# Kernel tuning notes

Measured on AMD Instinct MI355X. Metric: run time of the kernel, lower is better.

Reference implementation:

```python
import jax, jax.numpy as jnp
import numpy as np

N_, E_, A_, B_, H_, DH_ = 8000, 12000, 48000, 64, 64, 4096
STEPS, POOL_ITERS = 4, 3

def rbf(x, K, cutoff):
    mu = jnp.linspace(0.0, cutoff, K).astype(x.dtype)
    gamma = 1.0 / (cutoff / (K - 1)) ** 2
    return jnp.exp(-gamma * (x[..., None] - mu) ** 2)

def gru_step(x, h, Wih, Whh, bih, bhh):
    gi = x @ Wih.T + bih
    gh = h @ Whh.T + bhh
    ir, iz, inew = jnp.split(gi, 3, axis=-1)
    hr, hz, hnew = jnp.split(gh, 3, axis=-1)
    r = jax.nn.sigmoid(ir + hr)
    z = jax.nn.sigmoid(iz + hz)
    n = jnp.tanh(inew + r * hnew)
    return (1.0 - z) * n + z * h

def lstm_step(x, h, c, Wih, Whh, bih, bhh):
    g = x @ Wih.T + bih + h @ Whh.T + bhh
    i, f, gg, o = jnp.split(g, 4, axis=-1)
    c2 = jax.nn.sigmoid(f) * c + jax.nn.sigmoid(i) * jnp.tanh(gg)
    h2 = jax.nn.sigmoid(o) * jnp.tanh(c2)
    return h2, c2

def seg_softmax(e, seg, num_seg):
    m = jax.ops.segment_max(e, seg, num_segments=num_seg)
    ex = jnp.exp(e - m[seg])
    s = jax.ops.segment_sum(ex, seg, num_segments=num_seg)
    return ex / s[seg]

def _forward(node_attribute, edge_attribute, edge_length, angle, edge_src, edge_dst, angle_src, angle_dst, graph_ids, projW, projb, bondW, bondb, efW, efb, gnn_b, buW, bub, auW, aub, gWih, gWhh, gbih, gbhh, sWih0, sWhh0, sbih0, sbhh0, sWih1, sWhh1, sbih1, sbhh1, spW, spb, prelu_a):
    N, E = node_attribute.shape[0], edge_src.shape[0]
    x0 = jax.nn.relu(node_attribute @ projW + projb)  # [N, H]
    len_rbf = rbf(edge_length, 8, 4.0)                # [E, 8]
    edge_feat = jnp.concatenate([edge_attribute, len_rbf], axis=-1)  # [E, 16]
    ee_feat = jnp.concatenate([rbf(angle, 8, float(np.pi)), len_rbf[angle_src]], axis=-1)  # [A, 16]
    Wb = (edge_feat @ bondW + bondb).reshape(E, H_, H_)  # per-bond weight matrices (constant over steps)
    Wa = (ee_feat @ efW + efb).reshape(-1, H_, H_)       # per-angle weight matrices
    nf, hid = x0, x0
    for _ in range(STEPS):
        bm = nf[edge_src]                                # gather src node feats per bond [E, H]
        ha = jax.nn.relu(bm @ auW + aub)                 # angle_update
        m_ang = jnp.einsum('ai,aio->ao', ha[angle_src], Wa)  # [A, H]
        amsg = jax.ops.segment_sum(m_ang, angle_dst, num_segments=E)  # scatter-sum to bonds
        hb = jax.nn.relu(bm @ buW + bub) + amsg          # bond_update + angle message
        m = jnp.einsum('ei,eio->eo', hb, Wb)             # [E, H]
        nf = jax.nn.relu(jax.ops.segment_sum(m, edge_dst, num_segments=N) + gnn_b)
        nf = gru_step(nf, hid, gWih, gWhh, gbih, gbhh)   # 1-step, 1-layer GRU: output == new hidden
        hid = nf
    agg = jnp.concatenate([nf, x0], axis=-1)             # [N, 2H]
    D = agg.shape[-1]
    q_star = jnp.zeros((B_, 2 * D), agg.dtype)
    h0 = jnp.zeros((B_, D), agg.dtype); c0 = h0
    h1 = h0; c1 = h0
    for _ in range(POOL_ITERS):                          # Set2Set
        h0, c0 = lstm_step(q_star, h0, c0, sWih0, sWhh0, sbih0, sbhh0)
        h1, c1 = lstm_step(h0, h1, c1, sWih1, sWhh1, sbih1, sbhh1)
        q = h1                                           # [B, D]
        e = jnp.sum(agg * q[graph_ids], axis=-1)         # [N]
        alpha = seg_softmax(e, graph_ids, B_)
        readout = jax.ops.segment_sum(alpha[:, None] * agg, graph_ids, num_segments=B_)
        q_star = jnp.concatenate([q, readout], axis=-1)  # [B, 2D]
    out = q_star @ spW + spb                             # [B, DH]
    return jnp.where(out >= 0, out, prelu_a * out)       # PReLU

def setup_inputs():
    key = jax.random.key(0)
    ks = jax.random.split(key, 40)
    r = lambda i, shape, s=1.0: s * jax.random.normal(ks[i], shape, jnp.float32)
    inp = {}
    inp['node_attribute'] = r(0, (N_, 110))
    inp['edge_attribute'] = r(1, (E_, 8))
    inp['edge_length'] = jax.random.uniform(ks[2], (E_,), jnp.float32, 0.5, 4.0)
    inp['angle'] = jax.random.uniform(ks[3], (A_,), jnp.float32, 0.0, float(np.pi))
    inp['edge_src'] = jax.random.randint(ks[4], (E_,), 0, N_)
    inp['edge_dst'] = jax.random.randint(ks[5], (E_,), 0, N_)
    inp['angle_src'] = jax.random.randint(ks[6], (A_,), 0, E_)
    inp['angle_dst'] = jax.random.randint(ks[7], (A_,), 0, E_)
    inp['graph_ids'] = jnp.sort(jax.random.randint(ks[8], (N_,), 0, B_))
    w = 0.05
    inp['projW'] = r(9, (110, H_), w); inp['projb'] = jnp.zeros((H_,), jnp.float32)
    inp['bondW'] = r(10, (16, H_ * H_), w); inp['bondb'] = jnp.zeros((H_ * H_,), jnp.float32)
    inp['efW'] = r(11, (16, H_ * H_), w); inp['efb'] = jnp.zeros((H_ * H_,), jnp.float32)
    inp['gnn_b'] = jnp.zeros((H_,), jnp.float32)
    inp['buW'] = r(12, (H_, H_), w); inp['bub'] = jnp.zeros((H_,), jnp.float32)
    inp['auW'] = r(13, (H_, H_), w); inp['aub'] = jnp.zeros((H_,), jnp.float32)
    inp['gWih'] = r(14, (3 * H_, H_), w); inp['gWhh'] = r(15, (3 * H_, H_), w)
    inp['gbih'] = jnp.zeros((3 * H_,), jnp.float32); inp['gbhh'] = jnp.zeros((3 * H_,), jnp.float32)
    D = 2 * H_  # Set2Set feature dim = 128
    inp['sWih0'] = r(16, (4 * D, 2 * D), w); inp['sWhh0'] = r(17, (4 * D, D), w)
    inp['sbih0'] = jnp.zeros((4 * D,), jnp.float32); inp['sbhh0'] = jnp.zeros((4 * D,), jnp.float32)
    inp['sWih1'] = r(18, (4 * D, D), w); inp['sWhh1'] = r(19, (4 * D, D), w)
    inp['sbih1'] = jnp.zeros((4 * D,), jnp.float32); inp['sbhh1'] = jnp.zeros((4 * D,), jnp.float32)
    inp['spW'] = r(20, (4 * H_, DH_), w); inp['spb'] = jnp.zeros((DH_,), jnp.float32)
    inp['prelu_a'] = jnp.full((1,), 0.25, jnp.float32)
    return inp

def reference(node_attribute, edge_attribute, edge_length, angle, edge_src, edge_dst, angle_src, angle_dst, graph_ids, projW, projb, bondW, bondb, efW, efb, gnn_b, buW, bub, auW, aub, gWih, gWhh, gbih, gbhh, sWih0, sWhh0, sbih0, sbhh0, sWih1, sWhh1, sbih1, sbhh1, spW, spb, prelu_a):
    return _forward(node_attribute, edge_attribute, edge_length, angle, edge_src, edge_dst, angle_src, angle_dst, graph_ids, projW, projb, bondW, bondb, efW, efb, gnn_b, buW, bub, auW, aub, gWih, gWhh, gbih, gbhh, sWih0, sWhh0, sbih0, sbhh0, sWih1, sWhh1, sbih1, sbhh1, spW, spb, prelu_a)
```

## Files before the change

kernel.cpp:

```cpp
#include <hip/hip_runtime.h>
#include <math.h>

#define N_N 8000
#define N_E 12000
#define N_A 48000
#define N_B 64
#define N_H 64
#define N_DH 4096

typedef _Float16 h16;
typedef __attribute__((ext_vector_type(8))) _Float16 h16x8;
typedef __attribute__((ext_vector_type(4))) float f32x4;

__device__ __forceinline__ float atomAddF(float* p, float v) {
  return __hip_atomic_fetch_add(p, v, __ATOMIC_RELAXED, __HIP_MEMORY_SCOPE_AGENT);
}
__device__ __forceinline__ float sigm(float x) { return 1.f / (1.f + expf(-x)); }

#define SB_PROJ 2000
#define SB_FEAT (SB_PROJ + 235)
#define SB_PREP (SB_FEAT + 704)
#define SB_BND  (SB_PREP + 32)
#define SB_ZERO (SB_BND + 1330)
#define PREP_B0 32768
#define PREP_B1 (PREP_B0 + 69632)
#define PREP_B2 (PREP_B1 + 69632)
#define PREP_B3 (PREP_B2 + 4096)
#define PREP_B4 (PREP_B3 + 4096)

__global__ __launch_bounds__(256) void k_setup(
    const float* __restrict__ na, const float* __restrict__ projW,
    const float* __restrict__ projb, const float* __restrict__ ea,
    const float* __restrict__ el, const float* __restrict__ ang,
    const int* __restrict__ asrc, const int* __restrict__ gid,
    const float* __restrict__ gWih, const float* __restrict__ gWhh,
    const float* __restrict__ efW, const float* __restrict__ efb,
    const float* __restrict__ bondW, const float* __restrict__ bondb,
    const float* __restrict__ auW, const float* __restrict__ buW,
    float* __restrict__ x0, float* __restrict__ ef, float* __restrict__ ee,
    int* __restrict__ gstart, int* __restrict__ gend,
    h16* __restrict__ W3t, h16* __restrict__ ttA, h16* __restrict__ ttB,
    h16* __restrict__ wtAU, h16* __restrict__ wtBU,
    float4* __restrict__ amsg0_4, float4* __restrict__ nacc0_4,
    float4* __restrict__ qz_4) {
  int bx = blockIdx.x, tid = threadIdx.x;
  if (bx < SB_PROJ) {
    int wid = bx * 4 + (tid >> 6);
    int lane = tid & 63;
    if (wid < N_N) {
      const float* row = na + (size_t)wid * 110;
      float acc = projb[lane];
      for (int k = 0; k < 110; ++k) acc = fmaf(row[k], projW[k * 64 + lane], acc);
      x0[(size_t)wid * 64 + lane] = fmaxf(acc, 0.f);
    }
  } else if (bx < SB_FEAT) {
    int i = (bx - SB_PROJ) * 256 + tid;
    const float g2 = (7.f / 4.f) * (7.f / 4.f);
    if (i < N_E) {
      int e = i;
      float x = el[e];
#pragma unroll
      for (int j = 0; j < 8; ++j) ef[e * 16 + j] = ea[e * 8 + j];
#pragma unroll
      for (int j = 0; j < 8; ++j) {
        float d = x - j * (4.f / 7.f);
        ef[e * 16 + 8 + j] = expf(-g2 * d * d);
      }
    } else if (i < N_E + N_A) {
      int a = i - N_E;
      const float PIf = 3.14159265358979323846f;
      float x = ang[a];
      float g1 = (7.f / PIf) * (7.f / PIf);
#pragma unroll
      for (int j = 0; j < 8; ++j) {
        float d = x - j * (PIf / 7.f);
        ee[a * 16 + j] = expf(-g1 * d * d);
      }
      float y = el[asrc[a]];
#pragma unroll
      for (int j = 0; j < 8; ++j) {
        float d = y - j * (4.f / 7.f);
        ee[a * 16 + 8 + j] = expf(-g2 * d * d);
      }
    }
  } else if (bx < SB_PREP) {
    int i = (bx - SB_FEAT) * 256 + tid;
    if (i < PREP_B0) {
      int col = i >> 7, k = i & 127;
      int grp = col >> 6, u = col & 63;
      float v;
      if (grp == 0) v = (k < 64) ? gWih[u * 64 + k] : gWhh[u * 64 + k - 64];
      else if (grp == 1) v = (k < 64) ? gWih[(64 + u) * 64 + k] : gWhh[(64 + u) * 64 + k - 64];
      else if (grp == 2) v = (k < 64) ? gWih[(128 + u) * 64 + k] : 0.f;
      else v = (k < 64) ? 0.f : gWhh[(128 + u) * 64 + k - 64];
      W3t[i] = (h16)v;
    } else if (i < PREP_B1) {
      int j = i - PREP_B0;
      int n = j >> 6, i2 = j & 63;
      int k = n >> 6, o = n & 63;
      float val = (k < 16) ? efW[(size_t)k * 4096 + i2 * 64 + o] : efb[i2 * 64 + o];
      ttA[j] = (h16)val;
    } else if (i < PREP_B2) {
      int j = i - PREP_B1;
      int n = j >> 6, i2 = j & 63;
      int k = n >> 6, o = n & 63;
      float val = (k < 16) ? bondW[(size_t)k * 4096 + i2 * 64 + o] : bondb[i2 * 64 + o];
      ttB[j] = (h16)val;
    } else if (i < PREP_B3) {
      int j = i - PREP_B2;
      int o = j >> 6, i2 = j & 63;
      wtAU[j] = (h16)auW[i2 * 64 + o];
    } else if (i < PREP_B4) {
      int j = i - PREP_B3;
      int o = j >> 6, i2 = j & 63;
      wtBU[j] = (h16)buW[i2 * 64 + o];
    }
  } else if (bx < SB_BND) {
    int n = (bx - SB_PREP) * 256 + tid;
    if (n < N_N) {
      int g = gid[n];
      if (n == 0 || gid[n - 1] != g) gstart[g] = n;
      if (n == N_N - 1 || gid[n + 1] != g) gend[g] = n + 1;
    }
  } else if (bx < SB_ZERO) {
    int i = (bx - SB_BND) * 256 + tid;
    float4 z = (float4){0.f, 0.f, 0.f, 0.f};
    if (i < 192000) amsg0_4[i] = z;
    else if (i < 320000) nacc0_4[i - 192000] = z;
    else if (i < 340480) qz_4[i - 320000] = z;
  }
}

template <bool ANGLE>
__global__ __launch_bounds__(256) void k_fused_mm(
    const float* __restrict__ xcur, const int* __restrict__ map,
    const int* __restrict__ esrc, const h16* __restrict__ WtU,
    const float* __restrict__ biasU, const float* __restrict__ amsg_in,
    const float* __restrict__ feat, const h16* __restrict__ Tt,
    const int* __restrict__ dst, float* __restrict__ outacc, int T,
    float4* __restrict__ zbuf, int zcount4) {
  if (zbuf && blockIdx.y == 0) {
    int stride = gridDim.x * 256;
    for (int i = blockIdx.x * 256 + threadIdx.x; i < zcount4; i += stride)
      zbuf[i] = (float4){0.f, 0.f, 0.f, 0.f};
  }
  __shared__ h16 haT[4][2048];
  __shared__ float f_lds[128 * 17];
  __shared__ int dst_lds[128];
  int tid = threadIdx.x;
  int base = blockIdx.x * 128;
  int oc = blockIdx.y;
  for (int e = tid; e < 128 * 16; e += 256) {
    int il = e >> 4, k = e & 15;
    int g = base + il;
    if (g >= T) g = T - 1;
    f_lds[il * 17 + k] = feat[(size_t)g * 16 + k];
  }
  if (tid < 128) {
    int g = base + tid;
    if (g >= T) g = T - 1;
    dst_lds[tid] = dst[g];
  }
  __syncthreads();

  int wave = tid >> 6, lane = tid & 63;
  int l15 = lane & 15, lq = lane >> 4;
  int ibl = wave * 32;
  int ib0 = base + ibl;
  h16* myT = haT[wave];

  {
    h16x8 xafr[2][2];
#pragma unroll
    for (int s = 0; s < 2; ++s) {
      int item = ib0 + s * 16 + l15;
      if (item >= T) item = T - 1;
      int e = ANGLE ? map[item] : item;
      const float* vp = xcur + (size_t)esrc[e] * 64;
#pragma unroll
      for (int ks = 0; ks < 2; ++ks) {
        const float4* p = (const float4*)(vp + ks * 32 + 8 * lq);
        float4 v0 = p[0], v1 = p[1];
        h16x8 a;
        a[0] = (h16)v0.x; a[1] = (h16)v0.y; a[2] = (h16)v0.z; a[3] = (h16)v0.w;
        a[4] = (h16)v1.x; a[5] = (h16)v1.y; a[6] = (h16)v1.z; a[7] = (h16)v1.w;
        xafr[s][ks] = a;
      }
    }
    f32x4 aU[2][4];
#pragma unroll
    for (int s = 0; s < 2; ++s)
#pragma unroll
      for (int nt = 0; nt < 4; ++nt) aU[s][nt] = (f32x4){0.f, 0.f, 0.f, 0.f};
#pragma unroll
    for (int nt = 0; nt < 4; ++nt) {
#pragma unroll
      for (int ks = 0; ks < 2; ++ks) {
        h16x8 b = *(const h16x8*)(WtU + (size_t)(nt * 16 + l15) * 64 + ks * 32 + 8 * lq);
#pragma unroll
        for (int s = 0; s < 2; ++s)
          aU[s][nt] = __builtin_amdgcn_mfma_f32_16x16x32_f16(xafr[s][ks], b, aU[s][nt], 0, 0, 0);
      }
    }
#pragma unroll
    for (int s = 0; s < 2; ++s) {
#pragma unroll
      for (int nt = 0; nt < 4; ++nt) {
        int o = nt * 16 + l15;
        float bo = biasU[o];
#pragma unroll
        for (int r = 0; r < 4; ++r) {
          int row = s * 16 + lq * 4 + r;
          float val = fmaxf(aU[s][nt][r] + bo, 0.f);
          if (!ANGLE) {
            int item = ib0 + row;
            if (item >= T) item = T - 1;
            val += amsg_in[(size_t)item * 64 + o];
          }
          int idx = (((row * 64 + o) << 1) ^ ((row & 7) << 4)) >> 1;
          myT[idx] = (h16)val;
        }
      }
    }
  }

  h16x8 afr[2][2];
#pragma unroll
  for (int s = 0; s < 2; ++s) {
#pragma unroll
    for (int ks = 0; ks < 2; ++ks) {
      int row = s * 16 + l15;
      int byte = ((row * 64 + ks * 32 + 8 * lq) << 1) ^ ((row & 7) << 4);
      afr[s][ks] = *(const h16x8*)((const char*)myT + byte);
    }
  }

  f32x4 acc[2][2];
#pragma unroll
  for (int s = 0; s < 2; ++s)
#pragma unroll
    for (int nt = 0; nt < 2; ++nt) acc[s][nt] = (f32x4){0.f, 0.f, 0.f, 0.f};

  for (int kk = 0; kk < 16; ++kk) {
    h16x8 bfr[2][2];
#pragma unroll
    for (int nt = 0; nt < 2; ++nt)
#pragma unroll
      for (int ks = 0; ks < 2; ++ks)
        bfr[nt][ks] = *(const h16x8*)(Tt + (size_t)(kk * 64 + (oc * 2 + nt) * 16 + l15) * 64 +
                                      ks * 32 + 8 * lq);
    h16x8 a2[2][2];
#pragma unroll
    for (int s = 0; s < 2; ++s) {
      h16 fs = (h16)f_lds[(ibl + s * 16 + l15) * 17 + kk];
      a2[s][0] = afr[s][0] * fs;
      a2[s][1] = afr[s][1] * fs;
    }
#pragma unroll
    for (int s = 0; s < 2; ++s)
#pragma unroll
      for (int nt = 0; nt < 2; ++nt)
#pragma unroll
        for (int ks = 0; ks < 2; ++ks)
          acc[s][nt] = __builtin_amdgcn_mfma_f32_16x16x32_f16(a2[s][ks], bfr[nt][ks],
                                                              acc[s][nt], 0, 0, 0);
  }
  {
    h16x8 bfr[2][2];
#pragma unroll
    for (int nt = 0; nt < 2; ++nt)
#pragma unroll
      for (int ks = 0; ks < 2; ++ks)
        bfr[nt][ks] = *(const h16x8*)(Tt + (size_t)(16 * 64 + (oc * 2 + nt) * 16 + l15) * 64 +
                                      ks * 32 + 8 * lq);
#pragma unroll
    for (int s = 0; s < 2; ++s)
#pragma unroll
      for (int nt = 0; nt < 2; ++nt)
#pragma unroll
        for (int ks = 0; ks < 2; ++ks)
          acc[s][nt] = __builtin_amdgcn_mfma_f32_16x16x32_f16(afr[s][ks], bfr[nt][ks],
                                                              acc[s][nt], 0, 0, 0);
  }

#pragma unroll
  for (int s = 0; s < 2; ++s) {
#pragma unroll
    for (int r = 0; r < 4; ++r) {
      int il = ibl + s * 16 + lq * 4 + r;
      int item = base + il;
      if (item < T) {
        float* op = outacc + (size_t)dst_lds[il] * 64;
#pragma unroll
        for (int nt = 0; nt < 2; ++nt)
          atomAddF(op + (oc * 2 + nt) * 16 + l15, acc[s][nt][r]);
      }
    }
  }
}

__global__ __launch_bounds__(256) void k_gru2(
    const float* __restrict__ nacc, const float* __restrict__ gnnb,
    const float* __restrict__ h, const h16* __restrict__ W3t,
    const float* __restrict__ gbih, const float* __restrict__ gbhh,
    float* __restrict__ hout, const float* __restrict__ x0,
    float* __restrict__ agg, int wagg, float4* __restrict__ zbuf, int zcount4) {
  if (zbuf) {
    int stride = gridDim.x * 256;
    for (int i = blockIdx.x * 256 + threadIdx.x; i < zcount4; i += stride)
      zbuf[i] = (float4){0.f, 0.f, 0.f, 0.f};
  }
  int tid = threadIdx.x, wave = tid >> 6, lane = tid & 63;
  int l15 = lane & 15, lq = lane >> 4;
  int ib0 = blockIdx.x * 64 + wave * 16;
  int nodeA = ib0 + l15;
  if (nodeA >= N_N) nodeA = N_N - 1;

  h16x8 afr[4];
#pragma unroll
  for (int ks = 0; ks < 2; ++ks) {
    const float4* p = (const float4*)(nacc + (size_t)nodeA * 64 + ks * 32 + 8 * lq);
    const float4* gp = (const float4*)(gnnb + ks * 32 + 8 * lq);
    float4 v0 = p[0], v1 = p[1], g0 = gp[0], g1 = gp[1];
    h16x8 a;
    a[0] = (h16)fmaxf(v0.x + g0.x, 0.f); a[1] = (h16)fmaxf(v0.y + g0.y, 0.f);
    a[2] = (h16)fmaxf(v0.z + g0.z, 0.f); a[3] = (h16)fmaxf(v0.w + g0.w, 0.f);
    a[4] = (h16)fmaxf(v1.x + g1.x, 0.f); a[5] = (h16)fmaxf(v1.y + g1.y, 0.f);
    a[6] = (h16)fmaxf(v1.z + g1.z, 0.f); a[7] = (h16)fmaxf(v1.w + g1.w, 0.f);
    afr[ks] = a;
  }
#pragma unroll
  for (int ks = 0; ks < 2; ++ks) {
    const float4* p = (const float4*)(h + (size_t)nodeA * 64 + ks * 32 + 8 * lq);
    float4 v0 = p[0], v1 = p[1];
    h16x8 a;
    a[0] = (h16)v0.x; a[1] = (h16)v0.y; a[2] = (h16)v0.z; a[3] = (h16)v0.w;
    a[4] = (h16)v1.x; a[5] = (h16)v1.y; a[6] = (h16)v1.z; a[7] = (h16)v1.w;
    afr[2 + ks] = a;
  }

  f32x4 acc[16];
#pragma unroll
  for (int nt = 0; nt < 16; ++nt) acc[nt] = (f32x4){0.f, 0.f, 0.f, 0.f};
#pragma unroll
  for (int nt = 0; nt < 16; ++nt) {
#pragma unroll
    for (int ks = 0; ks < 4; ++ks) {
      if (nt >= 8 && nt < 12 && ks >= 2) continue;
      if (nt >= 12 && ks < 2) continue;
      h16x8 b = *(const h16x8*)(W3t + (size_t)(nt * 16 + l15) * 128 + ks * 32 + 8 * lq);
      acc[nt] = __builtin_amdgcn_mfma_f32_16x16x32_f16(afr[ks], b, acc[nt], 0, 0, 0);
    }
  }

#pragma unroll
  for (int nt0 = 0; nt0 < 4; ++nt0) {
    int u = nt0 * 16 + l15;
    float br = gbih[u] + gbhh[u];
    float bz = gbih[64 + u] + gbhh[64 + u];
    float bin_ = gbih[128 + u];
    float bhn = gbhh[128 + u];
#pragma unroll
    for (int r = 0; r < 4; ++r) {
      int node = ib0 + lq * 4 + r;
      if (node < N_N) {
        float rr = sigm(acc[nt0][r] + br);
        float zz = sigm(acc[nt0 + 4][r] + bz);
        float nn = tanhf(acc[nt0 + 8][r] + bin_ + rr * (acc[nt0 + 12][r] + bhn));
        float hv = h[(size_t)node * 64 + u];
        float val = (1.f - zz) * nn + zz * hv;
        hout[(size_t)node * 64 + u] = val;
        if (wagg) {
          agg[(size_t)node * 128 + u] = val;
          agg[(size_t)node * 128 + 64 + u] = x0[(size_t)node * 64 + u];
        }
      }
    }
  }
}


__global__ __launch_bounds__(256) void k_lstm2(
    const float* __restrict__ x, int xdim,
    const float* __restrict__ hin, const float* __restrict__ cin,
    const float* __restrict__ Wih, const float* __restrict__ Whh,
    const float* __restrict__ bih, const float* __restrict__ bhh,
    float* __restrict__ hout, float* __restrict__ cout) {
  int w = (blockIdx.x * blockDim.x + threadIdx.x) >> 6;
  int lane = threadIdx.x & 63;
  if (w >= N_B * 128) return;
  int b = w >> 7, u = w & 127;
  float a0 = 0.f, a1 = 0.f, a2 = 0.f, a3 = 0.f;
  const float* xr = x + (size_t)b * xdim;
  for (int k = lane; k < xdim; k += 64) {
    float xv = xr[k];
    a0 = fmaf(xv, Wih[(size_t)u * xdim + k], a0);
    a1 = fmaf(xv, Wih[(size_t)(128 + u) * xdim + k], a1);
    a2 = fmaf(xv, Wih[(size_t)(256 + u) * xdim + k], a2);
    a3 = fmaf(xv, Wih[(size_t)(384 + u) * xdim + k], a3);
  }
  const float* hr = hin + (size_t)b * 128;
#pragma unroll
  for (int k0 = 0; k0 < 128; k0 += 64) {
    int k = k0 + lane;
    float hv = hr[k];
    a0 = fmaf(hv, Whh[(size_t)u * 128 + k], a0);
    a1 = fmaf(hv, Whh[(size_t)(128 + u) * 128 + k], a1);
    a2 = fmaf(hv, Whh[(size_t)(256 + u) * 128 + k], a2);
    a3 = fmaf(hv, Whh[(size_t)(384 + u) * 128 + k], a3);
  }
#pragma unroll
  for (int m = 1; m < 64; m <<= 1) {
    a0 += __shfl_xor(a0, m);
    a1 += __shfl_xor(a1, m);
    a2 += __shfl_xor(a2, m);
    a3 += __shfl_xor(a3, m);
  }
  if (lane == 0) {
    float gi = a0 + bih[u] + bhh[u];
    float gf = a1 + bih[128 + u] + bhh[128 + u];
    float gg = a2 + bih[256 + u] + bhh[256 + u];
    float go = a3 + bih[384 + u] + bhh[384 + u];
    float c2 = sigm(gf) * cin[(size_t)b * 128 + u] + sigm(gi) * tanhf(gg);
    hout[(size_t)b * 128 + u] = sigm(go) * tanhf(c2);
    cout[(size_t)b * 128 + u] = c2;
  }
}

__global__ __launch_bounds__(256) void k_pool2(
    const float* __restrict__ agg, const int* __restrict__ gstart,
    const int* __restrict__ gend, const float* __restrict__ q,
    float* __restrict__ q_star) {
  int g = blockIdx.x;
  int s = gstart[g], t = gend[g];
  int cnt = t - s;
  if (cnt < 0) cnt = 0;
  if (cnt > 1024) cnt = 1024;
  __shared__ float ew[1024];
  __shared__ float red[8];
  __shared__ float comb[256];
  int tid = threadIdx.x, wave = tid >> 6, lane = tid & 63;
  float qa = q[g * 128 + lane], qb = q[g * 128 + 64 + lane];
  for (int i = wave; i < cnt; i += 4) {
    int n = s + i;
    float a = agg[(size_t)n * 128 + lane] * qa + agg[(size_t)n * 128 + 64 + lane] * qb;
#pragma unroll
    for (int m = 1; m < 64; m <<= 1) a += __shfl_xor(a, m);
    if (lane == 0) ew[i] = a;
  }
  __syncthreads();
  float mx = -INFINITY;
  for (int i = tid; i < cnt; i += 256) mx = fmaxf(mx, ew[i]);
#pragma unroll
  for (int m = 1; m < 64; m <<= 1) mx = fmaxf(mx, __shfl_xor(mx, m));
  if (lane == 0) red[wave] = mx;
  __syncthreads();
  mx = fmaxf(fmaxf(red[0], red[1]), fmaxf(red[2], red[3]));
  float sm = 0.f;
  for (int i = tid; i < cnt; i += 256) sm += expf(ew[i] - mx);
#pragma unroll
  for (int m = 1; m < 64; m <<= 1) sm += __shfl_xor(sm, m);
  if (lane == 0) red[4 + wave] = sm;
  __syncthreads();
  sm = red[4] + red[5] + red[6] + red[7];
  float inv = (sm > 0.f) ? 1.f / sm : 0.f;
  __syncthreads();
  for (int i = tid; i < cnt; i += 256) ew[i] = expf(ew[i] - mx) * inv;
  __syncthreads();
  int d = tid & 127, half = tid >> 7;
  float acc = 0.f;
  for (int i = half; i < cnt; i += 2)
    acc = fmaf(ew[i], agg[(size_t)(s + i) * 128 + d], acc);
  comb[tid] = acc;
  __syncthreads();
  if (half == 0) {
    float r2 = acc + comb[128 + tid];
    q_star[(size_t)g * 256 + d] = q[(size_t)g * 128 + d];
    q_star[(size_t)g * 256 + 128 + d] = r2;
  }
}

__global__ void k_out(const float* __restrict__ qs, const float* __restrict__ W,
                      const float* __restrict__ bias, const float* __restrict__ pa,
                      float* __restrict__ out) {
  int idx = blockIdx.x * blockDim.x + threadIdx.x;
  if (idx >= N_B * N_DH) return;
  int b = idx >> 12, d = idx & 4095;
  float acc = bias[d];
  const float* q = qs + (size_t)b * 256;
  for (int k = 0; k < 256; ++k) acc = fmaf(q[k], W[(size_t)k * 4096 + d], acc);
  float a = pa[0];
  out[idx] = acc >= 0.f ? acc : a * acc;
}

enum : size_t {
  OFF_X0 = 0,
  OFF_HA = OFF_X0 + (size_t)N_N * 64,
  OFF_HB = OFF_HA + (size_t)N_N * 64,
  OFF_EF = OFF_HB + (size_t)N_N * 64,
  OFF_EE = OFF_EF + (size_t)N_E * 16,
  OFF_AMSG0 = OFF_EE + (size_t)N_A * 16,
  OFF_AMSG1 = OFF_AMSG0 + (size_t)N_E * 64,
  OFF_NACC0 = OFF_AMSG1 + (size_t)N_E * 64,
  OFF_NACC1 = OFF_NACC0 + (size_t)N_N * 64,
  OFF_AGG = OFF_NACC1 + (size_t)N_N * 64,
  OFF_QSTAR = OFF_AGG + (size_t)N_N * 128,
  OFF_H0A = OFF_QSTAR + N_B * 256,
  OFF_H0B = OFF_H0A + N_B * 128,
  OFF_C0A = OFF_H0B + N_B * 128,
  OFF_C0B = OFF_C0A + N_B * 128,
  OFF_H1A = OFF_C0B + N_B * 128,
  OFF_H1B = OFF_H1A + N_B * 128,
  OFF_C1A = OFF_H1B + N_B * 128,
  OFF_C1B = OFF_C1A + N_B * 128,
  OFF_GSTART = OFF_C1B + N_B * 128,
  OFF_GEND = OFF_GSTART + N_B,
  OFF_TT_ANG = (OFF_GEND + N_B + 63) & ~(size_t)63,
  OFF_TT_BOND = OFF_TT_ANG + 34816,
  OFF_WT_AU = OFF_TT_BOND + 34816,
  OFF_WT_BU = OFF_WT_AU + 2048,
  OFF_W3T = OFF_WT_BU + 2048,
  WS_FLOATS = OFF_W3T + 16384
};

extern "C" void kernel_launch(void* const* d_in, const int* in_sizes, int n_in,
                              void* d_out, int out_size, void* d_ws, size_t ws_size,
                              hipStream_t stream) {
  (void)in_sizes; (void)n_in; (void)out_size; (void)ws_size;
  const float* na    = (const float*)d_in[0];
  const float* ea    = (const float*)d_in[1];
  const float* el    = (const float*)d_in[2];
  const float* ang   = (const float*)d_in[3];
  const int*   esrc  = (const int*)d_in[4];
  const int*   edst  = (const int*)d_in[5];
  const int*   asrc  = (const int*)d_in[6];
  const int*   adst  = (const int*)d_in[7];
  const int*   gid   = (const int*)d_in[8];
  const float* projW = (const float*)d_in[9];
  const float* projb = (const float*)d_in[10];
  const float* bondW = (const float*)d_in[11];
  const float* bondb = (const float*)d_in[12];
  const float* efW   = (const float*)d_in[13];
  const float* efb   = (const float*)d_in[14];
  const float* gnnb  = (const float*)d_in[15];
  const float* buW   = (const float*)d_in[16];
  const float* bub   = (const float*)d_in[17];
  const float* auW   = (const float*)d_in[18];
  const float* aub   = (const float*)d_in[19];
  const float* gWih  = (const float*)d_in[20];
  const float* gWhh  = (const float*)d_in[21];
  const float* gbih  = (const float*)d_in[22];
  const float* gbhh  = (const float*)d_in[23];
  const float* sWih0 = (const float*)d_in[24];
  const float* sWhh0 = (const float*)d_in[25];
  const float* sbih0 = (const float*)d_in[26];
  const float* sbhh0 = (const float*)d_in[27];
  const float* sWih1 = (const float*)d_in[28];
  const float* sWhh1 = (const float*)d_in[29];
  const float* sbih1 = (const float*)d_in[30];
  const float* sbhh1 = (const float*)d_in[31];
  const float* spW   = (const float*)d_in[32];
  const float* spb   = (const float*)d_in[33];
  const float* pa    = (const float*)d_in[34];
  float* out = (float*)d_out;
  float* ws = (float*)d_ws;

  float* x0    = ws + OFF_X0;
  float* hA    = ws + OFF_HA;
  float* hB    = ws + OFF_HB;
  float* ef    = ws + OFF_EF;
  float* ee    = ws + OFF_EE;
  float* amsg0 = ws + OFF_AMSG0;
  float* amsg1 = ws + OFF_AMSG1;
  float* nacc0 = ws + OFF_NACC0;
  float* nacc1 = ws + OFF_NACC1;
  float* agg   = ws + OFF_AGG;
  float* qstar = ws + OFF_QSTAR;
  float* h0a = ws + OFF_H0A; float* h0b = ws + OFF_H0B;
  float* c0a = ws + OFF_C0A; float* c0b = ws + OFF_C0B;
  float* h1a = ws + OFF_H1A; float* h1b = ws + OFF_H1B;
  float* c1a = ws + OFF_C1A; float* c1b = ws + OFF_C1B;
  int* gstart = (int*)(ws + OFF_GSTART);
  h16* ttA = (h16*)(ws + OFF_TT_ANG);
  h16* ttB = (h16*)(ws + OFF_TT_BOND);
  h16* wtAU = (h16*)(ws + OFF_WT_AU);
  h16* wtBU = (h16*)(ws + OFF_WT_BU);
  h16* w3t  = (h16*)(ws + OFF_W3T);

  hipMemsetAsync(gstart, 0x7f, 2 * N_B * sizeof(int), stream);
  k_setup<<<SB_ZERO, 256, 0, stream>>>(
      na, projW, projb, ea, el, ang, asrc, gid, gWih, gWhh, efW, efb, bondW, bondb,
      auW, buW, x0, ef, ee, gstart, gstart + N_B, w3t, ttA, ttB, wtAU, wtBU,
      (float4*)amsg0, (float4*)nacc0, (float4*)qstar);

  const float* cur = x0;
  float* bufs[2] = {hA, hB};
  float* amsgs[2] = {amsg0, amsg1};
  float* naccs[2] = {nacc0, nacc1};
  for (int s = 0; s < 4; ++s) {
    float* amsg_c = amsgs[s & 1];
    float* amsg_o = amsgs[(s + 1) & 1];
    float* nacc_c = naccs[s & 1];
    float* nacc_o = naccs[(s + 1) & 1];
    k_fused_mm<true><<<dim3((N_A + 127) / 128, 2), 256, 0, stream>>>(
        cur, asrc, esrc, wtAU, aub, nullptr, ee, ttA, adst, amsg_c, N_A,
        nullptr, 0);
    k_fused_mm<false><<<dim3((N_E + 127) / 128, 2), 256, 0, stream>>>(
        cur, nullptr, esrc, wtBU, bub, amsg_c, ef, ttB, edst, nacc_c, N_E,
        (float4*)amsg_o, N_E * 64 / 4);
    float* nxt = bufs[s & 1];
    k_gru2<<<(N_N + 63) / 64, 256, 0, stream>>>(nacc_c, gnnb, cur, w3t, gbih, gbhh,
                                                nxt, x0, agg, (s == 3) ? 1 : 0,
                                                (float4*)nacc_o, N_N * 64 / 4);
    cur = nxt;
  }

  float *h0i = h0a, *h0o = h0b, *c0i = c0a, *c0o = c0b;
  float *h1i = h1a, *h1o = h1b, *c1i = c1a, *c1o = c1b;
  for (int it = 0; it < 3; ++it) {
    k_lstm2<<<(N_B * 128 * 64 + 255) / 256, 256, 0, stream>>>(
        qstar, 256, h0i, c0i, sWih0, sWhh0, sbih0, sbhh0, h0o, c0o);
    k_lstm2<<<(N_B * 128 * 64 + 255) / 256, 256, 0, stream>>>(
        h0o, 128, h1i, c1i, sWih1, sWhh1, sbih1, sbhh1, h1o, c1o);
    k_pool2<<<N_B, 256, 0, stream>>>(agg, gstart, gstart + N_B, h1o, qstar);
    float* tmp;
    tmp = h0i; h0i = h0o; h0o = tmp;
    tmp = c0i; c0i = c0o; c0o = tmp;
    tmp = h1i; h1i = h1o; h1o = tmp;
    tmp = c1i; c1i = c1o; c1o = tmp;
  }
  k_out<<<(N_B * N_DH + 255) / 256, 256, 0, stream>>>(qstar, spW, spb, pa, out);
}
```

Baseline: 414.4 us.

## Factor angle messages per-edge, split bond kernel, fuse Set2Set into one kernel

```diff
diff --git a/kernel.cpp b/kernel.cpp
--- a/kernel.cpp
+++ b/kernel.cpp
@@ -18,31 +18,37 @@
 __device__ __forceinline__ float sigm(float x) { return 1.f / (1.f + expf(-x)); }
 
 #define SB_PROJ 2000
-#define SB_FEAT (SB_PROJ + 235)
-#define SB_PREP (SB_FEAT + 704)
+#define SB_FEAT (SB_PROJ + 47)
+#define SB_PREP (SB_FEAT + 1984)
 #define SB_BND  (SB_PREP + 32)
-#define SB_ZERO (SB_BND + 1330)
+#define SB_END  (SB_BND + 1250)
 #define PREP_B0 32768
 #define PREP_B1 (PREP_B0 + 69632)
 #define PREP_B2 (PREP_B1 + 69632)
 #define PREP_B3 (PREP_B2 + 4096)
 #define PREP_B4 (PREP_B3 + 4096)
+#define PREP_B5 (PREP_B4 + 131072)
+#define PREP_B6 (PREP_B5 + 65536)
+#define PREP_B7 (PREP_B6 + 65536)
+#define PREP_B8 (PREP_B7 + 65536)
 
 __global__ __launch_bounds__(256) void k_setup(
     const float* __restrict__ na, const float* __restrict__ projW,
     const float* __restrict__ projb, const float* __restrict__ ea,
-    const float* __restrict__ el, const float* __restrict__ ang,
-    const int* __restrict__ asrc, const int* __restrict__ gid,
+    const float* __restrict__ el, const int* __restrict__ gid,
     const float* __restrict__ gWih, const float* __restrict__ gWhh,
     const float* __restrict__ efW, const float* __restrict__ efb,
     const float* __restrict__ bondW, const float* __restrict__ bondb,
     const float* __restrict__ auW, const float* __restrict__ buW,
-    float* __restrict__ x0, float* __restrict__ ef, float* __restrict__ ee,
+    const float* __restrict__ sWih0, const float* __restrict__ sWhh0,
+    const float* __restrict__ sWih1, const float* __restrict__ sWhh1,
+    float* __restrict__ x0, float* __restrict__ ef,
     int* __restrict__ gstart, int* __restrict__ gend,
     h16* __restrict__ W3t, h16* __restrict__ ttA, h16* __restrict__ ttB,
     h16* __restrict__ wtAU, h16* __restrict__ wtBU,
-    float4* __restrict__ amsg0_4, float4* __restrict__ nacc0_4,
-    float4* __restrict__ qz_4) {
+    float* __restrict__ w0xT, float* __restrict__ w0hT,
+    float* __restrict__ w1xT, float* __restrict__ w1hT,
+    float4* __restrict__ amsg0_4, float4* __restrict__ nacc0_4) {
   int bx = blockIdx.x, tid = threadIdx.x;
   if (bx < SB_PROJ) {
     int wid = bx * 4 + (tid >> 6);
@@ -54,10 +60,9 @@
       x0[(size_t)wid * 64 + lane] = fmaxf(acc, 0.f);
     }
   } else if (bx < SB_FEAT) {
-    int i = (bx - SB_PROJ) * 256 + tid;
-    const float g2 = (7.f / 4.f) * (7.f / 4.f);
-    if (i < N_E) {
-      int e = i;
+    int e = (bx - SB_PROJ) * 256 + tid;
+    if (e < N_E) {
+      const float g2 = (7.f / 4.f) * (7.f / 4.f);
       float x = el[e];
 #pragma unroll
       for (int j = 0; j < 8; ++j) ef[e * 16 + j] = ea[e * 8 + j];
@@ -65,22 +70,6 @@
       for (int j = 0; j < 8; ++j) {
         float d = x - j * (4.f / 7.f);
         ef[e * 16 + 8 + j] = expf(-g2 * d * d);
-      }
-    } else if (i < N_E + N_A) {
-      int a = i - N_E;
-      const float PIf = 3.14159265358979323846f;
-      float x = ang[a];
-      float g1 = (7.f / PIf) * (7.f / PIf);
-#pragma unroll
-      for (int j = 0; j < 8; ++j) {
-        float d = x - j * (PIf / 7.f);
-        ee[a * 16 + j] = expf(-g1 * d * d);
-      }
-      float y = el[asrc[a]];
-#pragma unroll
-      for (int j = 0; j < 8; ++j) {
-        float d = y - j * (4.f / 7.f);
-        ee[a * 16 + 8 + j] = expf(-g2 * d * d);
       }
     }
   } else if (bx < SB_PREP) {
@@ -114,6 +103,22 @@
       int j = i - PREP_B3;
       int o = j >> 6, i2 = j & 63;
       wtBU[j] = (h16)buW[i2 * 64 + o];
+    } else if (i < PREP_B5) {
+      int j = i - PREP_B4;
+      int k = j >> 9, r = j & 511;
+      w0xT[j] = sWih0[(size_t)r * 256 + k];
+    } else if (i < PREP_B6) {
+      int j = i - PREP_B5;
+      int k = j >> 9, r = j & 511;
+      w0hT[j] = sWhh0[(size_t)r * 128 + k];
+    } else if (i < PREP_B7) {
+      int j = i - PREP_B6;
+      int k = j >> 9, r = j & 511;
+      w1xT[j] = sWih1[(size_t)r * 128 + k];
+    } else if (i < PREP_B8) {
+      int j = i - PREP_B7;
+      int k = j >> 9, r = j & 511;
+      w1hT[j] = sWhh1[(size_t)r * 128 + k];
     }
   } else if (bx < SB_BND) {
     int n = (bx - SB_PREP) * 256 + tid;
@@ -122,51 +127,35 @@
       if (n == 0 || gid[n - 1] != g) gstart[g] = n;
       if (n == N_N - 1 || gid[n + 1] != g) gend[g] = n + 1;
     }
-  } else if (bx < SB_ZERO) {
+  } else if (bx < SB_END) {
     int i = (bx - SB_BND) * 256 + tid;
     float4 z = (float4){0.f, 0.f, 0.f, 0.f};
     if (i < 192000) amsg0_4[i] = z;
     else if (i < 320000) nacc0_4[i - 192000] = z;
-    else if (i < 340480) qz_4[i - 320000] = z;
   }
 }
 
-template <bool ANGLE>
-__global__ __launch_bounds__(256) void k_fused_mm(
-    const float* __restrict__ xcur, const int* __restrict__ map,
-    const int* __restrict__ esrc, const h16* __restrict__ WtU,
-    const float* __restrict__ biasU, const float* __restrict__ amsg_in,
-    const float* __restrict__ feat, const h16* __restrict__ Tt,
-    const int* __restrict__ dst, float* __restrict__ outacc, int T,
-    float4* __restrict__ zbuf, int zcount4) {
-  if (zbuf && blockIdx.y == 0) {
-    int stride = gridDim.x * 256;
-    for (int i = blockIdx.x * 256 + threadIdx.x; i < zcount4; i += stride)
-      zbuf[i] = (float4){0.f, 0.f, 0.f, 0.f};
-  }
+__global__ __launch_bounds__(256) void k_edgeP(
+    const float* __restrict__ xcur, const int* __restrict__ esrc,
+    const h16* __restrict__ wtAU, const float* __restrict__ aub,
+    const h16* __restrict__ ttA, const float* __restrict__ ef,
+    h16* __restrict__ P8, float* __restrict__ Q) {
   __shared__ h16 haT[4][2048];
-  __shared__ float f_lds[128 * 17];
-  __shared__ int dst_lds[128];
-  int tid = threadIdx.x;
+  __shared__ float f_lds[128 * 9];
+  int tid = threadIdx.x, wave = tid >> 6, lane = tid & 63;
+  int l15 = lane & 15, lq = lane >> 4;
+  int oc = blockIdx.y;
   int base = blockIdx.x * 128;
-  int oc = blockIdx.y;
-  for (int e = tid; e < 128 * 16; e += 256) {
-    int il = e >> 4, k = e & 15;
-    int g = base + il;
-    if (g >= T) g = T - 1;
-    f_lds[il * 17 + k] = feat[(size_t)g * 16 + k];
-  }
-  if (tid < 128) {
-    int g = base + tid;
-    if (g >= T) g = T - 1;
-    dst_lds[tid] = dst[g];
-  }
-  __syncthreads();
-
-  int wave = tid >> 6, lane = tid & 63;
-  int l15 = lane & 15, lq = lane >> 4;
-  int ibl = wave * 32;
-  int ib0 = base + ibl;
+  if (oc >= 2) {
+    for (int e2 = tid; e2 < 128 * 8; e2 += 256) {
+      int il = e2 >> 3, k = e2 & 7;
+      int g = base + il;
+      if (g >= N_E) g = N_E - 1;
+      f_lds[il * 9 + k] = ef[(size_t)g * 16 + 8 + k];
+    }
+    __syncthreads();
+  }
+  int ibl = wave * 32, ib0 = base + ibl;
   h16* myT = haT[wave];
 
   {
@@ -174,9 +163,8 @@
 #pragma unroll
     for (int s = 0; s < 2; ++s) {
       int item = ib0 + s * 16 + l15;
-      if (item >= T) item = T - 1;
-      int e = ANGLE ? map[item] : item;
-      const float* vp = xcur + (size_t)esrc[e] * 64;
+      if (item >= N_E) item = N_E - 1;
+      const float* vp = xcur + (size_t)esrc[item] * 64;
 #pragma unroll
       for (int ks = 0; ks < 2; ++ks) {
         const float4* p = (const float4*)(vp + ks * 32 + 8 * lq);
@@ -193,62 +181,241 @@
 #pragma unroll
       for (int nt = 0; nt < 4; ++nt) aU[s][nt] = (f32x4){0.f, 0.f, 0.f, 0.f};
 #pragma unroll
-    for (int nt = 0; nt < 4; ++nt) {
+    for (int nt = 0; nt < 4; ++nt)
 #pragma unroll
       for (int ks = 0; ks < 2; ++ks) {
-        h16x8 b = *(const h16x8*)(WtU + (size_t)(nt * 16 + l15) * 64 + ks * 32 + 8 * lq);
+        h16x8 b = *(const h16x8*)(wtAU + (size_t)(nt * 16 + l15) * 64 + ks * 32 + 8 * lq);
 #pragma unroll
         for (int s = 0; s < 2; ++s)
           aU[s][nt] = __builtin_amdgcn_mfma_f32_16x16x32_f16(xafr[s][ks], b, aU[s][nt], 0, 0, 0);
       }
-    }
-#pragma unroll
-    for (int s = 0; s < 2; ++s) {
+#pragma unroll
+    for (int s = 0; s < 2; ++s)
 #pragma unroll
       for (int nt = 0; nt < 4; ++nt) {
         int o = nt * 16 + l15;
-        float bo = biasU[o];
+        float bo = aub[o];
 #pragma unroll
         for (int r = 0; r < 4; ++r) {
           int row = s * 16 + lq * 4 + r;
           float val = fmaxf(aU[s][nt][r] + bo, 0.f);
-          if (!ANGLE) {
-            int item = ib0 + row;
-            if (item >= T) item = T - 1;
-            val += amsg_in[(size_t)item * 64 + o];
-          }
           int idx = (((row * 64 + o) << 1) ^ ((row & 7) << 4)) >> 1;
           myT[idx] = (h16)val;
         }
       }
-    }
-  }
-
+  }
   h16x8 afr[2][2];
 #pragma unroll
-  for (int s = 0; s < 2; ++s) {
+  for (int s = 0; s < 2; ++s)
 #pragma unroll
     for (int ks = 0; ks < 2; ++ks) {
       int row = s * 16 + l15;
       int byte = ((row * 64 + ks * 32 + 8 * lq) << 1) ^ ((row & 7) << 4);
       afr[s][ks] = *(const h16x8*)((const char*)myT + byte);
     }
-  }
-
-  f32x4 acc[2][2];
+
+  if (oc < 2) {
+#pragma unroll
+    for (int kk = oc * 4; kk < oc * 4 + 4; ++kk) {
+      f32x4 acc[2][4];
+#pragma unroll
+      for (int s = 0; s < 2; ++s)
+#pragma unroll
+        for (int nt = 0; nt < 4; ++nt) acc[s][nt] = (f32x4){0.f, 0.f, 0.f, 0.f};
+#pragma unroll
+      for (int nt = 0; nt < 4; ++nt)
+#pragma unroll
+        for (int ks = 0; ks < 2; ++ks) {
+          h16x8 b = *(const h16x8*)(ttA + (size_t)(kk * 64 + nt * 16 + l15) * 64 +
+                                    ks * 32 + 8 * lq);
+#pragma unroll
+          for (int s = 0; s < 2; ++s)
+            acc[s][nt] = __builtin_amdgcn_mfma_f32_16x16x32_f16(afr[s][ks], b, acc[s][nt], 0, 0, 0);
+        }
+#pragma unroll
+      for (int s = 0; s < 2; ++s)
+#pragma unroll
+        for (int r = 0; r < 4; ++r) {
+          int e = ib0 + s * 16 + lq * 4 + r;
+          if (e < N_E) {
+#pragma unroll
+            for (int nt = 0; nt < 4; ++nt)
+              P8[((size_t)e * 8 + kk) * 64 + nt * 16 + l15] = (h16)acc[s][nt][r];
+          }
+        }
+    }
+  } else {
+    int no = oc - 2;
+    f32x4 qacc[2][2];
+#pragma unroll
+    for (int s = 0; s < 2; ++s)
+#pragma unroll
+      for (int nt = 0; nt < 2; ++nt) qacc[s][nt] = (f32x4){0.f, 0.f, 0.f, 0.f};
+    for (int kk = 8; kk < 16; ++kk) {
+      h16x8 a2[2][2];
+#pragma unroll
+      for (int s = 0; s < 2; ++s) {
+        h16 fs = (h16)f_lds[(ibl + s * 16 + l15) * 9 + (kk - 8)];
+        a2[s][0] = afr[s][0] * fs;
+        a2[s][1] = afr[s][1] * fs;
+      }
+#pragma unroll
+      for (int nt = 0; nt < 2; ++nt)
+#pragma unroll
+        for (int ks = 0; ks < 2; ++ks) {
+          h16x8 b = *(const h16x8*)(ttA + (size_t)(kk * 64 + (no * 2 + nt) * 16 + l15) * 64 +
+                                    ks * 32 + 8 * lq);
+#pragma unroll
+          for (int s = 0; s < 2; ++s)
+            qacc[s][nt] = __builtin_amdgcn_mfma_f32_16x16x32_f16(a2[s][ks], b, qacc[s][nt], 0, 0, 0);
+        }
+    }
+#pragma unroll
+    for (int nt = 0; nt < 2; ++nt)
+#pragma unroll
+      for (int ks = 0; ks < 2; ++ks) {
+        h16x8 b = *(const h16x8*)(ttA + (size_t)(16 * 64 + (no * 2 + nt) * 16 + l15) * 64 +
+                                  ks * 32 + 8 * lq);
+#pragma unroll
+        for (int s = 0; s < 2; ++s)
+          qacc[s][nt] = __builtin_amdgcn_mfma_f32_16x16x32_f16(afr[s][ks], b, qacc[s][nt], 0, 0, 0);
+      }
+#pragma unroll
+    for (int s = 0; s < 2; ++s)
+#pragma unroll
+      for (int r = 0; r < 4; ++r) {
+        int e = ib0 + s * 16 + lq * 4 + r;
+        if (e < N_E) {
+#pragma unroll
+          for (int nt = 0; nt < 2; ++nt)
+            Q[(size_t)e * 64 + (no * 2 + nt) * 16 + l15] = qacc[s][nt][r];
+        }
+      }
+  }
+}
+
+__global__ __launch_bounds__(256) void k_angle(
+    const float* __restrict__ ang, const int* __restrict__ asrc,
+    const int* __restrict__ adst, const h16* __restrict__ P8,
+    const float* __restrict__ Q, float* __restrict__ amsg) {
+  int w = (blockIdx.x * blockDim.x + threadIdx.x) >> 6;
+  int lane = threadIdx.x & 63;
+  if (w >= N_A) return;
+  float x = ang[w];
+  int e = asrc[w], d = adst[w];
+  float acc = Q[(size_t)e * 64 + lane];
+  const h16* p = P8 + (size_t)e * 512;
+  const float PIf = 3.14159265358979323846f;
+  const float g1 = (7.f / PIf) * (7.f / PIf);
+#pragma unroll
+  for (int j = 0; j < 8; ++j) {
+    float dd = x - j * (PIf / 7.f);
+    acc = fmaf(expf(-g1 * dd * dd), (float)p[j * 64 + lane], acc);
+  }
+  atomAddF(amsg + (size_t)d * 64 + lane, acc);
+}
+
+__global__ __launch_bounds__(256) void k_bond(
+    const float* __restrict__ xcur, const int* __restrict__ esrc,
+    const h16* __restrict__ wtBU, const float* __restrict__ bub,
+    const float* __restrict__ amsg_in, const float* __restrict__ ef,
+    const h16* __restrict__ ttB, const int* __restrict__ edst,
+    float* __restrict__ nacc, float4* __restrict__ zbuf, int zcount4) {
+  if (blockIdx.y == 0) {
+    int stride = gridDim.x * 256;
+    for (int i = blockIdx.x * 256 + threadIdx.x; i < zcount4; i += stride)
+      zbuf[i] = (float4){0.f, 0.f, 0.f, 0.f};
+  }
+  __shared__ h16 haT[4][2048];
+  __shared__ float f_lds[128 * 17];
+  __shared__ int dst_lds[128];
+  int tid = threadIdx.x;
+  int base = blockIdx.x * 128;
+  int oc = blockIdx.y;
+  for (int e2 = tid; e2 < 128 * 16; e2 += 256) {
+    int il = e2 >> 4, k = e2 & 15;
+    int g = base + il;
+    if (g >= N_E) g = N_E - 1;
+    f_lds[il * 17 + k] = ef[(size_t)g * 16 + k];
+  }
+  if (tid < 128) {
+    int g = base + tid;
+    if (g >= N_E) g = N_E - 1;
+    dst_lds[tid] = edst[g];
+  }
+  __syncthreads();
+
+  int wave = tid >> 6, lane = tid & 63;
+  int l15 = lane & 15, lq = lane >> 4;
+  int ibl = wave * 32, ib0 = base + ibl;
+  h16* myT = haT[wave];
+
+  {
+    h16x8 xafr[2][2];
+#pragma unroll
+    for (int s = 0; s < 2; ++s) {
+      int item = ib0 + s * 16 + l15;
+      if (item >= N_E) item = N_E - 1;
+      const float* vp = xcur + (size_t)esrc[item] * 64;
+#pragma unroll
+      for (int ks = 0; ks < 2; ++ks) {
+        const float4* p = (const float4*)(vp + ks * 32 + 8 * lq);
+        float4 v0 = p[0], v1 = p[1];
+        h16x8 a;
+        a[0] = (h16)v0.x; a[1] = (h16)v0.y; a[2] = (h16)v0.z; a[3] = (h16)v0.w;
+        a[4] = (h16)v1.x; a[5] = (h16)v1.y; a[6] = (h16)v1.z; a[7] = (h16)v1.w;
+        xafr[s][ks] = a;
+      }
+    }
+    f32x4 aU[2][4];
+#pragma unroll
+    for (int s = 0; s < 2; ++s)
+#pragma unroll
+      for (int nt = 0; nt < 4; ++nt) aU[s][nt] = (f32x4){0.f, 0.f, 0.f, 0.f};
+#pragma unroll
+    for (int nt = 0; nt < 4; ++nt)
+#pragma unroll
+      for (int ks = 0; ks < 2; ++ks) {
+        h16x8 b = *(const h16x8*)(wtBU + (size_t)(nt * 16 + l15) * 64 + ks * 32 + 8 * lq);
+#pragma unroll
+        for (int s = 0; s < 2; ++s)
+          aU[s][nt] = __builtin_amdgcn_mfma_f32_16x16x32_f16(xafr[s][ks], b, aU[s][nt], 0, 0, 0);
+      }
+#pragma unroll
+    for (int s = 0; s < 2; ++s)
+#pragma unroll
+      for (int nt = 0; nt < 4; ++nt) {
+        int o = nt * 16 + l15;
+        float bo = bub[o];
+#pragma unroll
+        for (int r = 0; r < 4; ++r) {
+          int row = s * 16 + lq * 4 + r;
+          int item = ib0 + row;
+          if (item >= N_E) item = N_E - 1;
+          float val = fmaxf(aU[s][nt][r] + bo, 0.f) + amsg_in[(size_t)item * 64 + o];
+          int idx = (((row * 64 + o) << 1) ^ ((row & 7) << 4)) >> 1;
+          myT[idx] = (h16)val;
+        }
+      }
+  }
+  h16x8 afr[2][2];
 #pragma unroll
   for (int s = 0; s < 2; ++s)
 #pragma unroll
-    for (int nt = 0; nt < 2; ++nt) acc[s][nt] = (f32x4){0.f, 0.f, 0.f, 0.f};
-
+    for (int ks = 0; ks < 2; ++ks) {
+      int row = s * 16 + l15;
+      int byte = ((row * 64 + ks * 32 + 8 * lq) << 1) ^ ((row & 7) << 4);
+      afr[s][ks] = *(const h16x8*)((const char*)myT + byte);
+    }
+
+  f32x4 acc[2];
+  acc[0] = (f32x4){0.f, 0.f, 0.f, 0.f};
+  acc[1] = (f32x4){0.f, 0.f, 0.f, 0.f};
   for (int kk = 0; kk < 16; ++kk) {
-    h16x8 bfr[2][2];
-#pragma unroll
-    for (int nt = 0; nt < 2; ++nt)
-#pragma unroll
-      for (int ks = 0; ks < 2; ++ks)
-        bfr[nt][ks] = *(const h16x8*)(Tt + (size_t)(kk * 64 + (oc * 2 + nt) * 16 + l15) * 64 +
-                                      ks * 32 + 8 * lq);
+    h16x8 bfr[2];
+#pragma unroll
+    for (int ks = 0; ks < 2; ++ks)
+      bfr[ks] = *(const h16x8*)(ttB + (size_t)(kk * 64 + oc * 16 + l15) * 64 + ks * 32 + 8 * lq);
     h16x8 a2[2][2];
 #pragma unroll
     for (int s = 0; s < 2; ++s) {
@@ -259,44 +426,29 @@
 #pragma unroll
     for (int s = 0; s < 2; ++s)
 #pragma unroll
-      for (int nt = 0; nt < 2; ++nt)
-#pragma unroll
-        for (int ks = 0; ks < 2; ++ks)
-          acc[s][nt] = __builtin_amdgcn_mfma_f32_16x16x32_f16(a2[s][ks], bfr[nt][ks],
-                                                              acc[s][nt], 0, 0, 0);
+      for (int ks = 0; ks < 2; ++ks)
+        acc[s] = __builtin_amdgcn_mfma_f32_16x16x32_f16(a2[s][ks], bfr[ks], acc[s], 0, 0, 0);
   }
   {
-    h16x8 bfr[2][2];
-#pragma unroll
-    for (int nt = 0; nt < 2; ++nt)
+    h16x8 bfr[2];
+#pragma unroll
+    for (int ks = 0; ks < 2; ++ks)
+      bfr[ks] = *(const h16x8*)(ttB + (size_t)(16 * 64 + oc * 16 + l15) * 64 + ks * 32 + 8 * lq);
+#pragma unroll
+    for (int s = 0; s < 2; ++s)
 #pragma unroll
       for (int ks = 0; ks < 2; ++ks)
-        bfr[nt][ks] = *(const h16x8*)(Tt + (size_t)(16 * 64 + (oc * 2 + nt) * 16 + l15) * 64 +
-                                      ks * 32 + 8 * lq);
-#pragma unroll
-    for (int s = 0; s < 2; ++s)
-#pragma unroll
-      for (int nt = 0; nt < 2; ++nt)
-#pragma unroll
-        for (int ks = 0; ks < 2; ++ks)
-          acc[s][nt] = __builtin_amdgcn_mfma_f32_16x16x32_f16(afr[s][ks], bfr[nt][ks],
-                                                              acc[s][nt], 0, 0, 0);
-  }
-
-#pragma unroll
-  for (int s = 0; s < 2; ++s) {
+        acc[s] = __builtin_amdgcn_mfma_f32_16x16x32_f16(afr[s][ks], bfr[ks], acc[s], 0, 0, 0);
+  }
+#pragma unroll
+  for (int s = 0; s < 2; ++s)
 #pragma unroll
     for (int r = 0; r < 4; ++r) {
       int il = ibl + s * 16 + lq * 4 + r;
       int item = base + il;
-      if (item < T) {
-        float* op = outacc + (size_t)dst_lds[il] * 64;
-#pragma unroll
-        for (int nt = 0; nt < 2; ++nt)
-          atomAddF(op + (oc * 2 + nt) * 16 + l15, acc[s][nt][r]);
-      }
-    }
-  }
+      if (item < N_E)
+        atomAddF(nacc + (size_t)dst_lds[il] * 64 + oc * 16 + l15, acc[s][r]);
+    }
 }
 
 __global__ __launch_bounds__(256) void k_gru2(
@@ -379,118 +531,133 @@
   }
 }
 
-
-__global__ __launch_bounds__(256) void k_lstm2(
-    const float* __restrict__ x, int xdim,
-    const float* __restrict__ hin, const float* __restrict__ cin,
-    const float* __restrict__ Wih, const float* __restrict__ Whh,
-    const float* __restrict__ bih, const float* __restrict__ bhh,
-    float* __restrict__ hout, float* __restrict__ cout) {
-  int w = (blockIdx.x * blockDim.x + threadIdx.x) >> 6;
-  int lane = threadIdx.x & 63;
-  if (w >= N_B * 128) return;
-  int b = w >> 7, u = w & 127;
-  float a0 = 0.f, a1 = 0.f, a2 = 0.f, a3 = 0.f;
-  const float* xr = x + (size_t)b * xdim;
-  for (int k = lane; k < xdim; k += 64) {
-    float xv = xr[k];
-    a0 = fmaf(xv, Wih[(size_t)u * xdim + k], a0);
-    a1 = fmaf(xv, Wih[(size_t)(128 + u) * xdim + k], a1);
-    a2 = fmaf(xv, Wih[(size_t)(256 + u) * xdim + k], a2);
-    a3 = fmaf(xv, Wih[(size_t)(384 + u) * xdim + k], a3);
-  }
-  const float* hr = hin + (size_t)b * 128;
-#pragma unroll
-  for (int k0 = 0; k0 < 128; k0 += 64) {
-    int k = k0 + lane;
-    float hv = hr[k];
-    a0 = fmaf(hv, Whh[(size_t)u * 128 + k], a0);
-    a1 = fmaf(hv, Whh[(size_t)(128 + u) * 128 + k], a1);
-    a2 = fmaf(hv, Whh[(size_t)(256 + u) * 128 + k], a2);
-    a3 = fmaf(hv, Whh[(size_t)(384 + u) * 128 + k], a3);
-  }
-#pragma unroll
-  for (int m = 1; m < 64; m <<= 1) {
-    a0 += __shfl_xor(a0, m);
-    a1 += __shfl_xor(a1, m);
-    a2 += __shfl_xor(a2, m);
-    a3 += __shfl_xor(a3, m);
-  }
-  if (lane == 0) {
-    float gi = a0 + bih[u] + bhh[u];
-    float gf = a1 + bih[128 + u] + bhh[128 + u];
-    float gg = a2 + bih[256 + u] + bhh[256 + u];
-    float go = a3 + bih[384 + u] + bhh[384 + u];
-    float c2 = sigm(gf) * cin[(size_t)b * 128 + u] + sigm(gi) * tanhf(gg);
-    hout[(size_t)b * 128 + u] = sigm(go) * tanhf(c2);
-    cout[(size_t)b * 128 + u] = c2;
-  }
-}
-
-__global__ __launch_bounds__(256) void k_pool2(
+__global__ __launch_bounds__(256) void k_s2s(
     const float* __restrict__ agg, const int* __restrict__ gstart,
-    const int* __restrict__ gend, const float* __restrict__ q,
-    float* __restrict__ q_star) {
-  int g = blockIdx.x;
+    const int* __restrict__ gend,
+    const float* __restrict__ w0xT, const float* __restrict__ w0hT,
+    const float* __restrict__ sbih0, const float* __restrict__ sbhh0,
+    const float* __restrict__ w1xT, const float* __restrict__ w1hT,
+    const float* __restrict__ sbih1, const float* __restrict__ sbhh1,
+    const float* __restrict__ spW, const float* __restrict__ spb,
+    const float* __restrict__ pa, float* __restrict__ out) {
+  int g = blockIdx.x, tid = threadIdx.x;
+  __shared__ float qs[256];
+  __shared__ float h0[128], c0[128], h1[128], c1[128];
+  __shared__ float gates[512];
+  __shared__ float ew[1024];
+  __shared__ float red[8];
+  __shared__ float comb[256];
+  if (tid < 256) qs[tid] = 0.f;
+  if (tid < 128) { h0[tid] = 0.f; c0[tid] = 0.f; h1[tid] = 0.f; c1[tid] = 0.f; }
   int s = gstart[g], t = gend[g];
   int cnt = t - s;
   if (cnt < 0) cnt = 0;
   if (cnt > 1024) cnt = 1024;
-  __shared__ float ew[1024];
-  __shared__ float red[8];
-  __shared__ float comb[256];
-  int tid = threadIdx.x, wave = tid >> 6, lane = tid & 63;
-  float qa = q[g * 128 + lane], qb = q[g * 128 + 64 + lane];
-  for (int i = wave; i < cnt; i += 4) {
-    int n = s + i;
-    float a = agg[(size_t)n * 128 + lane] * qa + agg[(size_t)n * 128 + 64 + lane] * qb;
-#pragma unroll
-    for (int m = 1; m < 64; m <<= 1) a += __shfl_xor(a, m);
-    if (lane == 0) ew[i] = a;
-  }
+  int wave = tid >> 6, lane = tid & 63;
   __syncthreads();
-  float mx = -INFINITY;
-  for (int i = tid; i < cnt; i += 256) mx = fmaxf(mx, ew[i]);
-#pragma unroll
-  for (int m = 1; m < 64; m <<= 1) mx = fmaxf(mx, __shfl_xor(mx, m));
-  if (lane == 0) red[wave] = mx;
-  __syncthreads();
-  mx = fmaxf(fmaxf(red[0], red[1]), fmaxf(red[2], red[3]));
-  float sm = 0.f;
-  for (int i = tid; i < cnt; i += 256) sm += expf(ew[i] - mx);
-#pragma unroll
-  for (int m = 1; m < 64; m <<= 1) sm += __shfl_xor(sm, m);
-  if (lane == 0) red[4 + wave] = sm;
-  __syncthreads();
-  sm = red[4] + red[5] + red[6] + red[7];
-  float inv = (sm > 0.f) ? 1.f / sm : 0.f;
-  __syncthreads();
-  for (int i = tid; i < cnt; i += 256) ew[i] = expf(ew[i] - mx) * inv;
-  __syncthreads();
-  int d = tid & 127, half = tid >> 7;
-  float acc = 0.f;
-  for (int i = half; i < cnt; i += 2)
-    acc = fmaf(ew[i], agg[(size_t)(s + i) * 128 + d], acc);
-  comb[tid] = acc;
-  __syncthreads();
-  if (half == 0) {
-    float r2 = acc + comb[128 + tid];
-    q_star[(size_t)g * 256 + d] = q[(size_t)g * 128 + d];
-    q_star[(size_t)g * 256 + 128 + d] = r2;
-  }
-}
-
-__global__ void k_out(const float* __restrict__ qs, const float* __restrict__ W,
-                      const float* __restrict__ bias, const float* __restrict__ pa,
-                      float* __restrict__ out) {
-  int idx = blockIdx.x * blockDim.x + threadIdx.x;
-  if (idx >= N_B * N_DH) return;
-  int b = idx >> 12, d = idx & 4095;
-  float acc = bias[d];
-  const float* q = qs + (size_t)b * 256;
-  for (int k = 0; k < 256; ++k) acc = fmaf(q[k], W[(size_t)k * 4096 + d], acc);
-  float a = pa[0];
-  out[idx] = acc >= 0.f ? acc : a * acc;
+
+  for (int it = 0; it < 3; ++it) {
+    {
+      int r0 = tid, r1 = tid + 256;
+      float a0 = sbih0[r0] + sbhh0[r0];
+      float a1 = sbih0[r1] + sbhh0[r1];
+      for (int k = 0; k < 256; ++k) {
+        float xv = qs[k];
+        a0 = fmaf(xv, w0xT[(size_t)k * 512 + r0], a0);
+        a1 = fmaf(xv, w0xT[(size_t)k * 512 + r1], a1);
+      }
+      for (int k = 0; k < 128; ++k) {
+        float hv = h0[k];
+        a0 = fmaf(hv, w0hT[(size_t)k * 512 + r0], a0);
+        a1 = fmaf(hv, w0hT[(size_t)k * 512 + r1], a1);
+      }
+      gates[r0] = a0;
+      gates[r1] = a1;
+    }
+    __syncthreads();
+    if (tid < 128) {
+      float gi = gates[tid], gf = gates[128 + tid], gg = gates[256 + tid], go = gates[384 + tid];
+      float c2 = sigm(gf) * c0[tid] + sigm(gi) * tanhf(gg);
+      c0[tid] = c2;
+      h0[tid] = sigm(go) * tanhf(c2);
+    }
+    __syncthreads();
+    {
+      int r0 = tid, r1 = tid + 256;
+      float a0 = sbih1[r0] + sbhh1[r0];
+      float a1 = sbih1[r1] + sbhh1[r1];
+      for (int k = 0; k < 128; ++k) {
+        float xv = h0[k], hv = h1[k];
+        a0 = fmaf(xv, w1xT[(size_t)k * 512 + r0], a0);
+        a1 = fmaf(xv, w1xT[(size_t)k * 512 + r1], a1);
+        a0 = fmaf(hv, w1hT[(size_t)k * 512 + r0], a0);
+        a1 = fmaf(hv, w1hT[(size_t)k * 512 + r1], a1);
+      }
+      gates[r0] = a0;
+      gates[r1] = a1;
+    }
+    __syncthreads();
+    if (tid < 128) {
+      float gi = gates[tid], gf = gates[128 + tid], gg = gates[256 + tid], go = gates[384 + tid];
+      float c2 = sigm(gf) * c1[tid] + sigm(gi) * tanhf(gg);
+      c1[tid] = c2;
+      h1[tid] = sigm(go) * tanhf(c2);
+    }
+    __syncthreads();
+    for (int i = wave; i < cnt; i += 4) {
+      int n = s + i;
+      float a = agg[(size_t)n * 128 + lane] * h1[lane] +
+                agg[(size_t)n * 128 + 64 + lane] * h1[64 + lane];
+#pragma unroll
+      for (int m = 1; m < 64; m <<= 1) a += __shfl_xor(a, m);
+      if (lane == 0) ew[i] = a;
+    }
+    __syncthreads();
+    float mx = -INFINITY;
+    for (int i = tid; i < cnt; i += 256) mx = fmaxf(mx, ew[i]);
+#pragma unroll
+    for (int m = 1; m < 64; m <<= 1) mx = fmaxf(mx, __shfl_xor(mx, m));
+    if (lane == 0) red[wave] = mx;
+    __syncthreads();
+    mx = fmaxf(fmaxf(red[0], red[1]), fmaxf(red[2], red[3]));
+    float sm = 0.f;
+    for (int i = tid; i < cnt; i += 256) sm += expf(ew[i] - mx);
+#pragma unroll
+    for (int m = 1; m < 64; m <<= 1) sm += __shfl_xor(sm, m);
+    if (lane == 0) red[4 + wave] = sm;
+    __syncthreads();
+    sm = red[4] + red[5] + red[6] + red[7];
+    float inv = (sm > 0.f) ? 1.f / sm : 0.f;
+    __syncthreads();
+    for (int i = tid; i < cnt; i += 256) ew[i] = expf(ew[i] - mx) * inv;
+    __syncthreads();
+    int d = tid & 127, half = tid >> 7;
+    float acc = 0.f;
+    for (int i = half; i < cnt; i += 2)
+      acc = fmaf(ew[i], agg[(size_t)(s + i) * 128 + d], acc);
+    comb[tid] = acc;
+    __syncthreads();
+    if (half == 0) {
+      qs[d] = h1[d];
+      qs[128 + d] = acc + comb[128 + tid];
+    }
+    __syncthreads();
+  }
+  float a_ = pa[0];
+  float oacc[16];
+#pragma unroll
+  for (int j = 0; j < 16; ++j) oacc[j] = spb[j * 256 + tid];
+  for (int k = 0; k < 256; ++k) {
+    float qv = qs[k];
+    const float* wr = spW + (size_t)k * 4096;
+#pragma unroll
+    for (int j = 0; j < 16; ++j) oacc[j] = fmaf(qv, wr[j * 256 + tid], oacc[j]);
+  }
+#pragma unroll
+  for (int j = 0; j < 16; ++j) {
+    float v = oacc[j];
+    out[(size_t)g * 4096 + j * 256 + tid] = v >= 0.f ? v : a_ * v;
+  }
 }
 
 enum : size_t {
@@ -498,29 +665,25 @@
   OFF_HA = OFF_X0 + (size_t)N_N * 64,
   OFF_HB = OFF_HA + (size_t)N_N * 64,
   OFF_EF = OFF_HB + (size_t)N_N * 64,
-  OFF_EE = OFF_EF + (size_t)N_E * 16,
-  OFF_AMSG0 = OFF_EE + (size_t)N_A * 16,
+  OFF_AMSG0 = OFF_EF + (size_t)N_E * 16,
   OFF_AMSG1 = OFF_AMSG0 + (size_t)N_E * 64,
   OFF_NACC0 = OFF_AMSG1 + (size_t)N_E * 64,
   OFF_NACC1 = OFF_NACC0 + (size_t)N_N * 64,
   OFF_AGG = OFF_NACC1 + (size_t)N_N * 64,
-  OFF_QSTAR = OFF_AGG + (size_t)N_N * 128,
-  OFF_H0A = OFF_QSTAR + N_B * 256,
-  OFF_H0B = OFF_H0A + N_B * 128,
-  OFF_C0A = OFF_H0B + N_B * 128,
-  OFF_C0B = OFF_C0A + N_B * 128,
-  OFF_H1A = OFF_C0B + N_B * 128,
-  OFF_H1B = OFF_H1A + N_B * 128,
-  OFF_C1A = OFF_H1B + N_B * 128,
-  OFF_C1B = OFF_C1A + N_B * 128,
-  OFF_GSTART = OFF_C1B + N_B * 128,
+  OFF_GSTART = OFF_AGG + (size_t)N_N * 128,
   OFF_GEND = OFF_GSTART + N_B,
   OFF_TT_ANG = (OFF_GEND + N_B + 63) & ~(size_t)63,
   OFF_TT_BOND = OFF_TT_ANG + 34816,
   OFF_WT_AU = OFF_TT_BOND + 34816,
   OFF_WT_BU = OFF_WT_AU + 2048,
   OFF_W3T = OFF_WT_BU + 2048,
-  WS_FLOATS = OFF_W3T + 16384
+  OFF_P8 = OFF_W3T + 16384,
+  OFF_Q = OFF_P8 + 3072000,
+  OFF_W0XT = OFF_Q + 768000,
+  OFF_W0HT = OFF_W0XT + 131072,
+  OFF_W1XT = OFF_W0HT + 65536,
+  OFF_W1HT = OFF_W1XT + 65536,
+  WS_FLOATS = OFF_W1HT + 65536
 };
 
 extern "C" void kernel_launch(void* const* d_in, const int* in_sizes, int n_in,
@@ -569,30 +732,31 @@
   float* hA    = ws + OFF_HA;
   float* hB    = ws + OFF_HB;
   float* ef    = ws + OFF_EF;
-  float* ee    = ws + OFF_EE;
   float* amsg0 = ws + OFF_AMSG0;
   float* amsg1 = ws + OFF_AMSG1;
   float* nacc0 = ws + OFF_NACC0;
   float* nacc1 = ws + OFF_NACC1;
   float* agg   = ws + OFF_AGG;
-  float* qstar = ws + OFF_QSTAR;
-  float* h0a = ws + OFF_H0A; float* h0b = ws + OFF_H0B;
-  float* c0a = ws + OFF_C0A; float* c0b = ws + OFF_C0B;
-  float* h1a = ws + OFF_H1A; float* h1b = ws + OFF_H1B;
-  float* c1a = ws + OFF_C1A; float* c1b = ws + OFF_C1B;
-  int* gstart = (int*)(ws + OFF_GSTART);
-  h16* ttA = (h16*)(ws + OFF_TT_ANG);
-  h16* ttB = (h16*)(ws + OFF_TT_BOND);
+  int* gstart  = (int*)(ws + OFF_GSTART);
+  h16* ttA  = (h16*)(ws + OFF_TT_ANG);
+  h16* ttB  = (h16*)(ws + OFF_TT_BOND);
   h16* wtAU = (h16*)(ws + OFF_WT_AU);
   h16* wtBU = (h16*)(ws + OFF_WT_BU);
   h16* w3t  = (h16*)(ws + OFF_W3T);
+  h16* P8   = (h16*)(ws + OFF_P8);
+  float* Q    = ws + OFF_Q;
+  float* w0xT = ws + OFF_W0XT;
+  float* w0hT = ws + OFF_W0HT;
+  float* w1xT = ws + OFF_W1XT;
+  float* w1hT = ws + OFF_W1HT;
 
   hipMemsetAsync(gstart, 0x7f, 2 * N_B * sizeof(int), stream);
-  k_setup<<<SB_ZERO, 256, 0, stream>>>(
-      na, projW, projb, ea, el, ang, asrc, gid, gWih, gWhh, efW, efb, bondW, bondb,
-      auW, buW, x0, ef, ee, gstart, gstart + N_B, w3t, ttA, ttB, wtAU, wtBU,
-      (float4*)amsg0, (float4*)nacc0, (float4*)qstar);
-
+  k_setup<<<SB_END, 256, 0, stream>>>(
+      na, projW, projb, ea, el, gid, gWih, gWhh, efW, efb, bondW, bondb, auW, buW,
+      sWih0, sWhh0, sWih1, sWhh1, x0, ef, gstart, gstart + N_B, w3t, ttA, ttB,
+      wtAU, wtBU, w0xT, w0hT, w1xT, w1hT, (float4*)amsg0, (float4*)nacc0);
+
+  const int EGX = (N_E + 127) / 128;
   const float* cur = x0;
   float* bufs[2] = {hA, hB};
   float* amsgs[2] = {amsg0, amsg1};
@@ -602,12 +766,11 @@
     float* amsg_o = amsgs[(s + 1) & 1];
     float* nacc_c = naccs[s & 1];
     float* nacc_o = naccs[(s + 1) & 1];
-    k_fused_mm<true><<<dim3((N_A + 127) / 128, 2), 256, 0, stream>>>(
-        cur, asrc, esrc, wtAU, aub, nullptr, ee, ttA, adst, amsg_c, N_A,
-        nullptr, 0);
-    k_fused_mm<false><<<dim3((N_E + 127) / 128, 2), 256, 0, stream>>>(
-        cur, nullptr, esrc, wtBU, bub, amsg_c, ef, ttB, edst, nacc_c, N_E,
-        (float4*)amsg_o, N_E * 64 / 4);
+    k_edgeP<<<dim3(EGX, 4), 256, 0, stream>>>(cur, esrc, wtAU, aub, ttA, ef, P8, Q);
+    k_angle<<<(N_A * 64) / 256, 256, 0, stream>>>(ang, asrc, adst, P8, Q, amsg_c);
+    k_bond<<<dim3(EGX, 4), 256, 0, stream>>>(cur, esrc, wtBU, bub, amsg_c, ef, ttB,
+                                             edst, nacc_c, (float4*)amsg_o,
+                                             N_E * 64 / 4);
     float* nxt = bufs[s & 1];
     k_gru2<<<(N_N + 63) / 64, 256, 0, stream>>>(nacc_c, gnnb, cur, w3t, gbih, gbhh,
                                                 nxt, x0, agg, (s == 3) ? 1 : 0,
@@ -615,19 +778,6 @@
     cur = nxt;
   }
 
-  float *h0i = h0a, *h0o = h0b, *c0i = c0a, *c0o = c0b;
-  float *h1i = h1a, *h1o = h1b, *c1i = c1a, *c1o = c1b;
-  for (int it = 0; it < 3; ++it) {
-    k_lstm2<<<(N_B * 128 * 64 + 255) / 256, 256, 0, stream>>>(
-        qstar, 256, h0i, c0i, sWih0, sWhh0, sbih0, sbhh0, h0o, c0o);
-    k_lstm2<<<(N_B * 128 * 64 + 255) / 256, 256, 0, stream>>>(
-        h0o, 128, h1i, c1i, sWih1, sWhh1, sbih1, sbhh1, h1o, c1o);
-    k_pool2<<<N_B, 256, 0, stream>>>(agg, gstart, gstart + N_B, h1o, qstar);
-    float* tmp;
-    tmp = h0i; h0i = h0o; h0o = tmp;
-    tmp = c0i; c0i = c0o; c0o = tmp;
-    tmp = h1i; h1i = h1o; h1o = tmp;
-    tmp = c1i; c1i = c1o; c1o = tmp;
-  }
-  k_out<<<(N_B * N_DH + 255) / 256, 256, 0, stream>>>(qstar, spW, spb, pa, out);
+  k_s2s<<<N_B, 256, 0, stream>>>(agg, gstart, gstart + N_B, w0xT, w0hT, sbih0, sbhh0,
+                                 w1xT, w1hT, sbih1, sbhh1, spW, spb, pa, out);
 }
```

Measured after the change: 442.1 us. 1.07x slower.
